# Performance work log

Measured on AMD Instinct MI355X. Metric: run time of the kernel, lower is better.

The kernel has to match this reference:

```python
import jax, jax.numpy as jnp
import numpy as np

NB = 8      # n_blocks
DIM = 256   # model dim (= context_len in source)
DI = 512    # dim_inner = dim * expand(2)
DCONV = 4   # depthwise conv kernel
NS = 16     # d_state
DTR = 16    # dt_rank = ceil(dim/16)
NE = 4      # experts
INNER = 512 # MoE FFN inner = dim * multi(2)
L = 8192    # sequence length
HOR = 32    # horizon
EPS = 1e-3


def setup_inputs() -> dict:
    key = jax.random.key(0)
    ks = jax.random.split(key, 16)
    s = 0.02
    f = lambda k, shp: jax.random.normal(k, shp, jnp.float32) * s
    return {
        "x": jax.random.normal(ks[0], (DIM, L), jnp.float32),
        "lin_w": f(ks[1], (DIM, DIM)),                      # shared by self.linear and self.out (tied)
        "in_proj_w": f(ks[2], (NB, 2 * DI, DIM)),
        "conv_w": f(ks[3], (NB, DI, 1, DCONV)),             # depthwise conv, groups=DI
        "conv_b": f(ks[4], (NB, DI)),
        "x_proj_w": f(ks[5], (NB, DTR + 2 * NS, DI)),
        "dt_proj_w": f(ks[6], (NB, DI, DTR)),
        "dt_proj_b": f(ks[7], (NB, DI)),
        "A_log": jnp.tile(jnp.log(jnp.arange(1, NS + 1, dtype=jnp.float32)), (NB, DI, 1)),
        "D_param": jnp.ones((NB, DI), jnp.float32),
        "out_proj_w": f(ks[8], (NB, DIM, DI)),
        "gate_w": f(ks[9], (NB, NE, DIM)),
        "gproj_w": f(ks[10], (NB, NE, INNER, DIM)),
        "uproj_w": f(ks[11], (NB, NE, INNER, DIM)),
        "dproj_w": f(ks[12], (NB, NE, DIM, INNER)),
        "rms_a_w": jnp.ones((DIM,), jnp.float32),
        "rms_f_w": jnp.ones((DIM,), jnp.float32),
        "head_w1": f(ks[13], (DIM, DIM)),
        "head_w2": f(ks[14], (HOR, DIM)),
    }


def _rmsnorm(h, w):
    return w * (h * jax.lax.rsqrt(jnp.mean(h * h, axis=-1, keepdims=True) + EPS))


def _mamba(h, ipw, cw, cb, xpw, dtw, dtb, alog, dpar, opw):
    b = h.shape[0]
    xr = jnp.einsum('bld,od->bol', h, ipw)            # (b, 2*DI, l)
    xc, res = jnp.split(xr, 2, axis=1)                # each (b, DI, l)
    # causal depthwise conv (padding=DCONV-1, sliced to length l)
    xc = jax.lax.conv_general_dilated(xc, cw, (1,), [(DCONV - 1, 0)],
                                      feature_group_count=DI,
                                      dimension_numbers=('NCH', 'OIH', 'NCH'))
    xc = jax.nn.silu(xc + cb[None, :, None])
    A = -jnp.exp(alog)                                # (DI, NS)
    xdbl = jnp.einsum('bdl,kd->blk', xc, xpw)         # (b, l, DTR+2*NS)
    dr, B, C = xdbl[..., :DTR], xdbl[..., DTR:DTR + NS], xdbl[..., DTR + NS:]
    delta = jax.nn.softplus(jnp.einsum('blr,dr->bld', dr, dtw) + dtb)
    dA = jnp.exp(jnp.einsum('bld,dn->lbdn', delta, A))          # (l, b, DI, NS)
    dBu = jnp.einsum('bld,bln,bdl->lbdn', delta, B, xc)         # (l, b, DI, NS)
    Cl = jnp.transpose(C, (1, 0, 2))                             # (l, b, NS)
    def step(carry, inp):
        a, bu, c = inp
        carry = a * carry + bu
        return carry, jnp.einsum('bdn,bn->bd', carry, c)
    _, ys = jax.lax.scan(step, jnp.zeros((b, DI, NS), xc.dtype), (dA, dBu, Cl))
    y = jnp.transpose(ys, (1, 2, 0)) + xc * dpar[:, None]        # (b, DI, l)
    y = y * jax.nn.silu(res)
    return jnp.einsum('bdl,od->blo', y, opw)                     # (b, l, DIM)


def _moe(h, gw, gp, up, dp):
    shp = h.shape
    xf = h.reshape(-1, shp[-1])                       # (T, DIM)
    scores = xf @ gw.T                                # (T, NE)
    vals, idx = jax.lax.top_k(scores, 2)
    w = jax.nn.softmax(vals, axis=-1)                 # (T, 2)
    g = jax.nn.silu(jnp.einsum('td,ehd->teh', xf, gp))
    u = jnp.einsum('td,ehd->teh', xf, up)
    eo = jnp.einsum('teh,edh->ted', g * u, dp)        # (T, NE, DIM)
    we = jnp.sum(w[..., None] * jax.nn.one_hot(idx, NE, dtype=xf.dtype), axis=1)  # (T, NE)
    return jnp.einsum('te,ted->td', we, eo).reshape(shp)


def reference(x, lin_w, in_proj_w, conv_w, conv_b, x_proj_w, dt_proj_w, dt_proj_b,
              A_log, D_param, out_proj_w, gate_w, gproj_w, uproj_w, dproj_w,
              rms_a_w, rms_f_w, head_w1, head_w2):
    h = x.T[None]                                     # (1, L, DIM)
    h = h @ lin_w.T
    for i in range(NB):
        resi = h
        h = _rmsnorm(h, rms_a_w)
        h = _mamba(h, in_proj_w[i], conv_w[i], conv_b[i], x_proj_w[i],
                   dt_proj_w[i], dt_proj_b[i], A_log[i], D_param[i], out_proj_w[i])
        h = h + resi
        resi = h
        h = _moe(h, gate_w[i], gproj_w[i], uproj_w[i], dproj_w[i])
        h = _rmsnorm(h, rms_f_w)
        h = h + resi
    h = h @ lin_w.T                                   # self.out (tied weight)
    h = jax.nn.silu(h @ head_w1.T) @ head_w2.T        # head
    return jax.nn.sigmoid(h[0].T)                     # (HOR, L)
```

## Files before the change

### kernel.cpp

```cpp
#include <hip/hip_runtime.h>

typedef unsigned short u16;
typedef unsigned int u32;
using bf16x8 = __attribute__((ext_vector_type(8))) short;
using f32x4 = __attribute__((ext_vector_type(4))) float;

constexpr int kL = 8192;
constexpr int kDIM = 256;
constexpr int kDI = 512;
constexpr int kNB = 8;
constexpr float kEPS = 1e-3f;

__device__ __forceinline__ u16 f2b(float f) {
  u32 x = __builtin_bit_cast(u32, f);
  x += 0x7fffu + ((x >> 16) & 1u);
  return (u16)(x >> 16);
}
__device__ __forceinline__ float b2f(u16 u) {
  return __builtin_bit_cast(float, (u32)u << 16);
}
__device__ __forceinline__ float sigm(float x) { return 1.f / (1.f + __expf(-x)); }
__device__ __forceinline__ float softplus_fast(float x) {
  return fmaxf(x, 0.f) + __logf(1.f + __expf(-fabsf(x)));
}

__device__ __forceinline__ void async_cp16(const void* g, void* l) {
  __builtin_amdgcn_global_load_lds((const __attribute__((address_space(1))) u32*)g,
                                   (__attribute__((address_space(3))) u32*)l, 16, 0, 0);
}

struct Cvt2 {
  const float* s[23];
  u16* d[23];
  int n[23];
  int mode[23];
  int bstart[24];
  int nseg;
};
__global__ __launch_bounds__(256) void cvt2_k(Cvt2 dd) {
  const int b = blockIdx.x;
  int seg = 0;
  for (int i = 1; i < dd.nseg; ++i) seg += (b >= dd.bstart[i]) ? 1 : 0;
  const int lb = b - dd.bstart[seg];
  const float* s = dd.s[seg];
  u16* d = dd.d[seg];
  const int n = dd.n[seg];
  const int mode = dd.mode[seg];
  #pragma unroll
  for (int it = 0; it < 4; ++it) {
    const int e4 = lb * 1024 + it * 256 + threadIdx.x;
    const int i = e4 * 4;
    if (i >= n) break;
    const float4 v = ((const float4*)s)[e4];
    ushort4 o = make_ushort4(f2b(v.x), f2b(v.y), f2b(v.z), f2b(v.w));
    size_t dst;
    if (mode == 0) {
      dst = (size_t)i;
    } else if (mode == 1) {
      const int row = i >> 8, col = i & 255;
      const int drow = (row >> 9) * 1024 + ((row >> 4) & 31) * 32 + (row & 15);
      dst = (size_t)drow * 256 + col;
    } else {
      const int bb = i >> 19, e = (i >> 17) & 3, nr = (i >> 9) & 255, j = i & 511;
      dst = (size_t)bb * 524288 + (size_t)nr * 2048 + e * 512 + j;
    }
    *(ushort4*)&d[dst] = o;
  }
}

__global__ __launch_bounds__(256) void transpose_x_k(const float* __restrict__ x, u16* __restrict__ xT) {
  __shared__ float tile[32][33];
  int l0 = blockIdx.x * 32, d0 = blockIdx.y * 32;
  int tx = threadIdx.x, ty = threadIdx.y;
  #pragma unroll
  for (int i = 0; i < 32; i += 8)
    tile[ty + i][tx] = x[(size_t)(d0 + ty + i) * kL + l0 + tx];
  __syncthreads();
  #pragma unroll
  for (int i = 0; i < 32; i += 8)
    xT[(size_t)(l0 + ty + i) * kDIM + d0 + tx] = f2b(tile[tx][ty + i]);
}

template <int BM, int BN, int TR, int TC, int WCN, int MODE>
__global__ __launch_bounds__(256) void gemm_t(
    const u16* __restrict__ A, int lda,
    const u16* __restrict__ W, int ldw,
    void* __restrict__ C, int ldc,
    int N, int K, int pstride)
{
  constexpr int BNR = (BN + 63) & ~63;
  __shared__ u16 As[BM * 64];
  __shared__ u16 Bs[BNR * 64];
  const int tid = threadIdx.x;
  const int lane = tid & 63;
  const int wave = tid >> 6;
  const int bm = blockIdx.x * BM;
  const int bn = blockIdx.y * BN;
  const int wrow = (wave / WCN) * (TR * 16);
  const int wcol = (wave % WCN) * (TC * 16);
  const int kchunk = K / (int)gridDim.z;
  const int kbeg = blockIdx.z * kchunk;
  const int kend = kbeg + kchunk;

  f32x4 acc[TR][TC];
  #pragma unroll
  for (int r = 0; r < TR; ++r)
    #pragma unroll
    for (int c = 0; c < TC; ++c)
      acc[r][c] = f32x4{0.f, 0.f, 0.f, 0.f};

  for (int k0 = kbeg; k0 < kend; k0 += 64) {
    #pragma unroll
    for (int it = 0; it < BM * 64 / 2048; ++it) {
      int flat = (it * 256 + tid) * 8;
      int r = flat >> 6;
      int gc = ((((flat >> 3) & 7) ^ (r & 7)) << 3);
      async_cp16(A + (size_t)(bm + r) * lda + k0 + gc, &As[flat]);
    }
    #pragma unroll
    for (int it = 0; it < BNR * 64 / 2048; ++it) {
      int flat = (it * 256 + tid) * 8;
      int r = flat >> 6;
      int gc = ((((flat >> 3) & 7) ^ (r & 7)) << 3);
      int n = bn + r;
      if (n > N - 1) n = N - 1;
      async_cp16(W + (size_t)n * ldw + k0 + gc, &Bs[flat]);
    }
    __syncthreads();
    #pragma unroll
    for (int kk = 0; kk < 64; kk += 32) {
      const int kc = (kk >> 3) + (lane >> 4);
      const int mrow = lane & 15;
      bf16x8 a[TR], b[TC];
      #pragma unroll
      for (int rr = 0; rr < TR; ++rr) {
        int row = wrow + rr * 16 + mrow;
        a[rr] = *(const bf16x8*)&As[row * 64 + ((kc ^ (row & 7)) << 3)];
      }
      #pragma unroll
      for (int cc = 0; cc < TC; ++cc) {
        int row = wcol + cc * 16 + mrow;
        b[cc] = *(const bf16x8*)&Bs[row * 64 + ((kc ^ (row & 7)) << 3)];
      }
      #pragma unroll
      for (int rr = 0; rr < TR; ++rr)
        #pragma unroll
        for (int cc = 0; cc < TC; ++cc)
          acc[rr][cc] = __builtin_amdgcn_mfma_f32_16x16x32_bf16(a[rr], b[cc], acc[rr][cc], 0, 0, 0);
    }
    __syncthreads();
  }

  const int colb = bn + wcol + (lane & 15);
  const int rowb = bm + wrow + ((lane >> 4) << 2);
  #pragma unroll
  for (int rr = 0; rr < TR; ++rr)
    #pragma unroll
    for (int cc = 0; cc < TC; ++cc) {
      int col = colb + cc * 16;
      if (col >= N) continue;
      #pragma unroll
      for (int i = 0; i < 4; ++i) {
        const int row = rowb + rr * 16 + i;
        size_t off = (size_t)row * ldc + col;
        float v = acc[rr][cc][i];
        if constexpr (MODE == 0) ((float*)C)[off] = v;
        else if constexpr (MODE == 2) ((u16*)C)[off] = f2b(v);
        else if constexpr (MODE == 3) ((u16*)C)[off] = f2b(v * sigm(v));
        else if constexpr (MODE == 4) atomicAdd(&((float*)C)[off], v);
        else if constexpr (MODE == 5) ((float*)C)[off + (size_t)blockIdx.z * pstride] = v;
        else if constexpr (MODE == 7) ((float*)C)[(size_t)col * kL + row] = sigm(v);
      }
    }
}

__global__ __launch_bounds__(512, 1) void moe_mega_k(
    float* __restrict__ h, const float* __restrict__ hpart,
    const float* __restrict__ gw,
    const u16* __restrict__ Wgu, const u16* __restrict__ Wd,
    const float* __restrict__ wf, const float* __restrict__ wa,
    u16* __restrict__ hb2, u16* __restrict__ hn)
{
  __shared__ u16 Ah[32 * 256];
  __shared__ u16 Ts[32 * 512];
  __shared__ u16 Ws[2][256 * 64];
  __shared__ float WeS[32][4];
  const int tid = threadIdx.x;
  const int lane = tid & 63;
  const int quad = lane >> 4;
  const int m16 = lane & 15;
  const int wave = tid >> 6;
  const int wcol = wave * 32;
  const int r0 = blockIdx.x * 32;
  const int prow = tid >> 4;
  const int pcol = (tid & 15) * 16;

  float hv[16];
  {
    const size_t base = (size_t)(r0 + prow) * 256 + pcol;
    #pragma unroll
    for (int j = 0; j < 16; j += 4) {
      float4 v = *(const float4*)(h + base + j);
      #pragma unroll
      for (int z = 0; z < 4; ++z) {
        const float4 pv = *(const float4*)(hpart + (size_t)z * 2097152 + base + j);
        v.x += pv.x; v.y += pv.y; v.z += pv.z; v.w += pv.w;
      }
      hv[j] = v.x; hv[j + 1] = v.y; hv[j + 2] = v.z; hv[j + 3] = v.w;
    }
  }
  {
    float p[4];
    #pragma unroll
    for (int e = 0; e < 4; ++e) {
      float s = 0.f;
      #pragma unroll
      for (int j = 0; j < 16; ++j) s += hv[j] * gw[e * 256 + pcol + j];
      p[e] = s;
    }
    #pragma unroll
    for (int o = 8; o > 0; o >>= 1) {
      p[0] += __shfl_xor(p[0], o); p[1] += __shfl_xor(p[1], o);
      p[2] += __shfl_xor(p[2], o); p[3] += __shfl_xor(p[3], o);
    }
    if ((tid & 15) == 0) {
      int i0 = 0;
      #pragma unroll
      for (int e = 1; e < 4; ++e) if (p[e] > p[i0]) i0 = e;
      int i1 = -1;
      #pragma unroll
      for (int e = 0; e < 4; ++e) {
        if (e == i0) continue;
        if (i1 < 0 || p[e] > p[i1]) i1 = e;
      }
      const float tt = __expf(p[i1] - p[i0]);
      float o0 = 1.f / (1.f + tt), o1 = tt / (1.f + tt);
      WeS[prow][0] = 0.f; WeS[prow][1] = 0.f; WeS[prow][2] = 0.f; WeS[prow][3] = 0.f;
      WeS[prow][i0] = o0; WeS[prow][i1] = o1;
    }
    #pragma unroll
    for (int cc = 0; cc < 2; ++cc) {
      const int chunk = (pcol >> 3) + cc;
      const int sw = ((chunk ^ (prow & 7)) << 3);
      u16 tmp[8];
      #pragma unroll
      for (int j = 0; j < 8; ++j) tmp[j] = f2b(hv[cc * 8 + j]);
      *(bf16x8*)&Ah[prow * 256 + sw] = *(bf16x8*)tmp;
    }
  }
  __syncthreads();

  f32x4 macc[2][2];
  #pragma unroll
  for (int rt = 0; rt < 2; ++rt)
    #pragma unroll
    for (int ct = 0; ct < 2; ++ct) macc[rt][ct] = f32x4{0.f, 0.f, 0.f, 0.f};

  auto stage_gu = [&](int buf, int e, int nc, int k0) {
    #pragma unroll
    for (int it = 0; it < 4; ++it) {
      const int flat = (it * 512 + tid) * 8;
      const int r = flat >> 6;
      const int gc = ((((flat >> 3) & 7) ^ (r & 7)) << 3);
      async_cp16(Wgu + (size_t)(e * 1024 + nc * 256 + r) * 256 + k0 + gc, &Ws[buf][flat]);
    }
  };
  auto stage_dp = [&](int buf, int e, int k0) {
    #pragma unroll
    for (int it = 0; it < 4; ++it) {
      const int flat = (it * 512 + tid) * 8;
      const int r = flat >> 6;
      const int gc = ((((flat >> 3) & 7) ^ (r & 7)) << 3);
      async_cp16(Wd + (size_t)r * 2048 + e * 512 + k0 + gc, &Ws[buf][flat]);
    }
  };

  for (int e = 0; e < 4; ++e) {
    for (int nc = 0; nc < 4; ++nc) {
      f32x4 acc[2][2];
      #pragma unroll
      for (int rt = 0; rt < 2; ++rt)
        #pragma unroll
        for (int ct = 0; ct < 2; ++ct) acc[rt][ct] = f32x4{0.f, 0.f, 0.f, 0.f};
      stage_gu(0, e, nc, 0);
      __syncthreads();
      #pragma unroll
      for (int k0i = 0; k0i < 4; ++k0i) {
        if (k0i < 3) stage_gu((k0i + 1) & 1, e, nc, (k0i + 1) * 64);
        const u16* buf = Ws[k0i & 1];
        #pragma unroll
        for (int kk = 0; kk < 64; kk += 32) {
          const int kcs = (kk >> 3) + quad;
          bf16x8 a[2], b[2];
          #pragma unroll
          for (int rt = 0; rt < 2; ++rt) {
            const int row = rt * 16 + m16;
            const int ch = ((k0i * 64 + kk) >> 3) + quad;
            a[rt] = *(const bf16x8*)&Ah[row * 256 + ((ch ^ (row & 7)) << 3)];
          }
          #pragma unroll
          for (int ct = 0; ct < 2; ++ct) {
            const int n = wcol + ct * 16 + m16;
            b[ct] = *(const bf16x8*)&buf[n * 64 + ((kcs ^ (n & 7)) << 3)];
          }
          #pragma unroll
          for (int rt = 0; rt < 2; ++rt)
            #pragma unroll
            for (int ct = 0; ct < 2; ++ct)
              acc[rt][ct] = __builtin_amdgcn_mfma_f32_16x16x32_bf16(a[rt], b[ct], acc[rt][ct], 0, 0, 0);
        }
        __syncthreads();
      }
      const int group = nc * 8 + wave;
      const int j = group * 16 + m16;
      #pragma unroll
      for (int rt = 0; rt < 2; ++rt)
        #pragma unroll
        for (int i = 0; i < 4; ++i) {
          const int row = rt * 16 + quad * 4 + i;
          const float g = acc[rt][0][i];
          const float u = acc[rt][1][i];
          const float val = g * sigm(g) * u * WeS[row][e];
          Ts[row * 512 + (((j >> 3) ^ (row & 7)) << 3) + (j & 7)] = f2b(val);
        }
    }
    __syncthreads();
    stage_dp(0, e, 0);
    __syncthreads();
    #pragma unroll
    for (int k0i = 0; k0i < 8; ++k0i) {
      if (k0i < 7) stage_dp((k0i + 1) & 1, e, (k0i + 1) * 64);
      const u16* buf = Ws[k0i & 1];
      #pragma unroll
      for (int kk = 0; kk < 64; kk += 32) {
        const int kcs = (kk >> 3) + quad;
        bf16x8 a[2], b[2];
        #pragma unroll
        for (int rt = 0; rt < 2; ++rt) {
          const int row = rt * 16 + m16;
          const int ch = ((k0i * 64 + kk) >> 3) + quad;
          a[rt] = *(const bf16x8*)&Ts[row * 512 + ((ch ^ (row & 7)) << 3)];
        }
        #pragma unroll
        for (int ct = 0; ct < 2; ++ct) {
          const int n = wcol + ct * 16 + m16;
          b[ct] = *(const bf16x8*)&buf[n * 64 + ((kcs ^ (n & 7)) << 3)];
        }
        #pragma unroll
        for (int rt = 0; rt < 2; ++rt)
          #pragma unroll
          for (int ct = 0; ct < 2; ++ct)
            macc[rt][ct] = __builtin_amdgcn_mfma_f32_16x16x32_bf16(a[rt], b[ct], macc[rt][ct], 0, 0, 0);
      }
      __syncthreads();
    }
  }

  float* MoeS = (float*)Ts;
  __syncthreads();
  #pragma unroll
  for (int rt = 0; rt < 2; ++rt)
    #pragma unroll
    for (int ct = 0; ct < 2; ++ct)
      #pragma unroll
      for (int i = 0; i < 4; ++i)
        MoeS[(rt * 16 + quad * 4 + i) * 256 + wcol + ct * 16 + m16] = macc[rt][ct][i];
  __syncthreads();

  float mv[16];
  float ss = 0.f;
  #pragma unroll
  for (int j = 0; j < 16; ++j) {
    mv[j] = MoeS[prow * 256 + pcol + j];
    ss += mv[j] * mv[j];
  }
  #pragma unroll
  for (int o = 8; o > 0; o >>= 1) ss += __shfl_xor(ss, o);
  const float r1 = rsqrtf(ss * (1.f / 256.f) + kEPS);
  float ss2 = 0.f;
  #pragma unroll
  for (int j = 0; j < 16; ++j) {
    hv[j] += wf[pcol + j] * mv[j] * r1;
    ss2 += hv[j] * hv[j];
  }
  #pragma unroll
  for (int o = 8; o > 0; o >>= 1) ss2 += __shfl_xor(ss2, o);
  const float r2 = rsqrtf(ss2 * (1.f / 256.f) + kEPS);

  const size_t base = (size_t)(r0 + prow) * 256 + pcol;
  #pragma unroll
  for (int j = 0; j < 16; j += 4)
    *(float4*)(h + base + j) = float4{hv[j], hv[j + 1], hv[j + 2], hv[j + 3]};
  #pragma unroll
  for (int j = 0; j < 16; j += 4) {
    *(ushort4*)(hb2 + base + j) = make_ushort4(f2b(hv[j]), f2b(hv[j + 1]), f2b(hv[j + 2]), f2b(hv[j + 3]));
    *(ushort4*)(hn + base + j) = make_ushort4(
        f2b(wa[pcol + j] * hv[j] * r2), f2b(wa[pcol + j + 1] * hv[j + 1] * r2),
        f2b(wa[pcol + j + 2] * hv[j + 2] * r2), f2b(wa[pcol + j + 3] * hv[j + 3] * r2));
  }
}

__device__ __forceinline__ float block_sum256(float v) {
  #pragma unroll
  for (int o = 32; o > 0; o >>= 1) v += __shfl_down(v, o);
  __shared__ float red[4];
  __syncthreads();
  if ((threadIdx.x & 63) == 0) red[threadIdx.x >> 6] = v;
  __syncthreads();
  return red[0] + red[1] + red[2] + red[3];
}

__global__ __launch_bounds__(256) void rms_a_k(const float* __restrict__ h, const float* __restrict__ w,
                                               u16* __restrict__ hn) {
  const int l = blockIdx.x, t = threadIdx.x;
  const float v = h[(size_t)l * kDIM + t];
  const float ssum = block_sum256(v * v);
  const float r = rsqrtf(ssum * (1.f / 256.f) + kEPS);
  hn[(size_t)l * kDIM + t] = f2b(w[t] * v * r);
}

__global__ __launch_bounds__(256) void conv_silu_k(const u16* __restrict__ xz, const float* __restrict__ cw,
                                                   const float* __restrict__ cb,
                                                   u16* __restrict__ xcb, u16* __restrict__ zsb,
                                                   float* __restrict__ xdbl) {
  const int i4 = blockIdx.x * 256 + threadIdx.x;
  if (i4 < 98304) *(float4*)&xdbl[i4 * 4] = float4{0.f, 0.f, 0.f, 0.f};
  const int l = i4 >> 7;
  const int d = (i4 & 127) * 4;
  float acc[4];
  const float4 cbv = *(const float4*)&cb[d];
  acc[0] = cbv.x; acc[1] = cbv.y; acc[2] = cbv.z; acc[3] = cbv.w;
  #pragma unroll
  for (int j = 0; j < 4; ++j) {
    const int ll = l - 3 + j;
    if (ll >= 0) {
      const ushort4 xv = *(const ushort4*)&xz[(size_t)ll * 1024 + d];
      acc[0] += cw[(d + 0) * 4 + j] * b2f(xv.x);
      acc[1] += cw[(d + 1) * 4 + j] * b2f(xv.y);
      acc[2] += cw[(d + 2) * 4 + j] * b2f(xv.z);
      acc[3] += cw[(d + 3) * 4 + j] * b2f(xv.w);
    }
  }
  ushort4 xo, zo;
  const ushort4 zv = *(const ushort4*)&xz[(size_t)l * 1024 + 512 + d];
  float z0 = b2f(zv.x), z1 = b2f(zv.y), z2 = b2f(zv.z), z3 = b2f(zv.w);
  xo.x = f2b(acc[0] * sigm(acc[0])); xo.y = f2b(acc[1] * sigm(acc[1]));
  xo.z = f2b(acc[2] * sigm(acc[2])); xo.w = f2b(acc[3] * sigm(acc[3]));
  zo.x = f2b(z0 * sigm(z0)); zo.y = f2b(z1 * sigm(z1));
  zo.z = f2b(z2 * sigm(z2)); zo.w = f2b(z3 * sigm(z3));
  *(ushort4*)&xcb[(size_t)l * 512 + d] = xo;
  *(ushort4*)&zsb[(size_t)l * 512 + d] = zo;
}

__global__ __launch_bounds__(256) void scan_a_k(const float* __restrict__ xdbl, const u16* __restrict__ xcb,
                                                const float* __restrict__ A_log, const float* __restrict__ dtw,
                                                const float* __restrict__ dtb,
                                                u16* __restrict__ delta,
                                                float* __restrict__ aprod, float* __restrict__ bacc) {
  const int c = blockIdx.x;
  const int t = threadIdx.x;
  const int half = t & 1;
  const int d = blockIdx.y * 128 + (t >> 1);
  const int l0 = c * 64;
  __shared__ float Xs[64][32];
  for (int i = t; i < 2048; i += 256)
    Xs[i >> 5][i & 31] = xdbl[(size_t)(l0 + (i >> 5)) * 48 + (i & 31)];
  __syncthreads();
  float wd[8], Ad[8];
  #pragma unroll
  for (int j = 0; j < 8; ++j) wd[j] = dtw[d * 16 + half * 8 + j];
  const float bd = dtb[d];
  #pragma unroll
  for (int n = 0; n < 8; ++n) Ad[n] = -__expf(A_log[d * 16 + half * 8 + n]);
  float s[8], ap[8];
  #pragma unroll
  for (int n = 0; n < 8; ++n) { s[n] = 0.f; ap[n] = 1.f; }
  #pragma unroll 4
  for (int lr = 0; lr < 64; ++lr) {
    const float4 dr0 = *(const float4*)&Xs[lr][half * 8];
    const float4 dr1 = *(const float4*)&Xs[lr][half * 8 + 4];
    float p0 = dr0.x * wd[0] + dr0.y * wd[1] + dr0.z * wd[2] + dr0.w * wd[3];
    float p1 = dr1.x * wd[4] + dr1.y * wd[5] + dr1.z * wd[6] + dr1.w * wd[7];
    float dot = p0 + p1;
    dot += __shfl_xor(dot, 1);
    const float dl = softplus_fast(dot + bd);
    const int l = l0 + lr;
    if (!half) delta[(size_t)l * 512 + d] = f2b(dl);
    const float du = dl * b2f(xcb[(size_t)l * 512 + d]);
    const float4 B0 = *(const float4*)&Xs[lr][16 + half * 8];
    const float4 B1 = *(const float4*)&Xs[lr][16 + half * 8 + 4];
    const float Bv[8] = {B0.x, B0.y, B0.z, B0.w, B1.x, B1.y, B1.z, B1.w};
    #pragma unroll
    for (int n = 0; n < 8; ++n) {
      const float a = __expf(dl * Ad[n]);
      s[n] = fmaf(a, s[n], du * Bv[n]);
      ap[n] *= a;
    }
  }
  const int base = c * 8192 + d * 16 + half * 8;
  #pragma unroll
  for (int n = 0; n < 8; ++n) { aprod[base + n] = ap[n]; bacc[base + n] = s[n]; }
}

__global__ __launch_bounds__(256) void scan_b_k(const float* __restrict__ aprod, const float* __restrict__ bacc,
                                                float* __restrict__ sinit) {
  const int st = blockIdx.x * 256 + threadIdx.x;
  float cur = 0.f;
  float a0 = aprod[st], b0 = bacc[st];
  for (int c = 0; c < 128; ++c) {
    float a1 = 0.f, b1 = 0.f;
    if (c + 1 < 128) {
      a1 = aprod[(size_t)(c + 1) * 8192 + st];
      b1 = bacc[(size_t)(c + 1) * 8192 + st];
    }
    sinit[(size_t)c * 8192 + st] = cur;
    cur = fmaf(a0, cur, b0);
    a0 = a1; b0 = b1;
  }
}

__global__ __launch_bounds__(256) void scan_c_k(const float* __restrict__ xdbl, const u16* __restrict__ xcb,
                                                const u16* __restrict__ zsb, const float* __restrict__ A_log,
                                                const u16* __restrict__ delta,
                                                const float* __restrict__ sinit,
                                                const float* __restrict__ Dp, u16* __restrict__ yv) {
  const int c = blockIdx.x;
  const int t = threadIdx.x;
  const int half = t & 1;
  const int d = blockIdx.y * 128 + (t >> 1);
  const int l0 = c * 64;
  __shared__ float Xs[64][32];
  for (int i = t; i < 2048; i += 256)
    Xs[i >> 5][i & 31] = xdbl[(size_t)(l0 + (i >> 5)) * 48 + 16 + (i & 31)];
  __syncthreads();
  float Ad[8];
  #pragma unroll
  for (int n = 0; n < 8; ++n) Ad[n] = -__expf(A_log[d * 16 + half * 8 + n]);
  float s[8];
  const int base = c * 8192 + d * 16 + half * 8;
  #pragma unroll
  for (int n = 0; n < 8; ++n) s[n] = sinit[base + n];
  const float Dd = Dp[d];
  #pragma unroll 4
  for (int lr = 0; lr < 64; ++lr) {
    const int l = l0 + lr;
    const float dl = b2f(delta[(size_t)l * 512 + d]);
    const float xv = b2f(xcb[(size_t)l * 512 + d]);
    const float zs = b2f(zsb[(size_t)l * 512 + d]);
    const float du = dl * xv;
    const float4 B0 = *(const float4*)&Xs[lr][half * 8];
    const float4 B1 = *(const float4*)&Xs[lr][half * 8 + 4];
    const float4 C0 = *(const float4*)&Xs[lr][16 + half * 8];
    const float4 C1 = *(const float4*)&Xs[lr][16 + half * 8 + 4];
    const float Bv[8] = {B0.x, B0.y, B0.z, B0.w, B1.x, B1.y, B1.z, B1.w};
    const float Cv[8] = {C0.x, C0.y, C0.z, C0.w, C1.x, C1.y, C1.z, C1.w};
    float y = 0.f;
    #pragma unroll
    for (int n = 0; n < 8; ++n) {
      const float a = __expf(dl * Ad[n]);
      s[n] = fmaf(a, s[n], du * Bv[n]);
      y = fmaf(s[n], Cv[n], y);
    }
    y += __shfl_xor(y, 1);
    if (!half) yv[(size_t)l * 512 + d] = f2b((y + xv * Dd) * zs);
  }
}

extern "C" void kernel_launch(void* const* d_in, const int* in_sizes, int n_in,
                              void* d_out, int out_size, void* d_ws, size_t ws_size,
                              hipStream_t stream) {
  const float* x        = (const float*)d_in[0];
  const float* lin_w    = (const float*)d_in[1];
  const float* in_proj  = (const float*)d_in[2];
  const float* conv_w   = (const float*)d_in[3];
  const float* conv_b   = (const float*)d_in[4];
  const float* x_proj   = (const float*)d_in[5];
  const float* dt_w     = (const float*)d_in[6];
  const float* dt_b     = (const float*)d_in[7];
  const float* A_log    = (const float*)d_in[8];
  const float* D_param  = (const float*)d_in[9];
  const float* out_proj = (const float*)d_in[10];
  const float* gate_w   = (const float*)d_in[11];
  const float* gproj    = (const float*)d_in[12];
  const float* uproj    = (const float*)d_in[13];
  const float* dproj    = (const float*)d_in[14];
  const float* rms_a_w  = (const float*)d_in[15];
  const float* rms_f_w  = (const float*)d_in[16];
  const float* head_w1  = (const float*)d_in[17];
  const float* head_w2  = (const float*)d_in[18];

  char* p = (char*)d_ws;
  auto alloc = [&](size_t bytes) -> char* {
    char* r = p;
    p += (bytes + 255) & ~(size_t)255;
    return r;
  };

  u16* lin_b  = (u16*)alloc(65536 * 2);
  u16* ipw_b  = (u16*)alloc((size_t)2097152 * 2);
  u16* xpw_b  = (u16*)alloc((size_t)196608 * 2);
  u16* opw_b  = (u16*)alloc((size_t)1048576 * 2);
  u16* gupw_b = (u16*)alloc((size_t)8388608 * 2);
  u16* dpw_b  = (u16*)alloc((size_t)4194304 * 2);
  u16* hw1_b  = (u16*)alloc(65536 * 2);
  u16* hw2_b  = (u16*)alloc(8192 * 2);

  u16* xT     = (u16*)alloc((size_t)kL * kDIM * 2);
  float* h    = (float*)alloc((size_t)kL * kDIM * 4);
  u16* hn     = (u16*)alloc((size_t)kL * kDIM * 2);
  u16* hb2    = (u16*)alloc((size_t)kL * kDIM * 2);
  float* xdbl = (float*)alloc((size_t)kL * 48 * 4);
  u16* fb     = (u16*)alloc((size_t)kL * kDIM * 2);
  u16* h2b    = (u16*)alloc((size_t)kL * kDIM * 2);
  u16* xz     = (u16*)alloc((size_t)kL * 1024 * 2);
  u16* xcb    = (u16*)alloc((size_t)kL * kDI * 2);
  u16* zsb    = (u16*)alloc((size_t)kL * kDI * 2);
  u16* yv     = (u16*)alloc((size_t)kL * kDI * 2);
  u16* delta  = (u16*)alloc((size_t)kL * kDI * 2);
  float* aprod = (float*)alloc((size_t)128 * 8192 * 4);
  float* bacc  = (float*)alloc((size_t)128 * 8192 * 4);
  float* sinit = (float*)alloc((size_t)128 * 8192 * 4);
  float* hpart = (float*)alloc((size_t)4 * kL * kDIM * 4);

  if ((size_t)(p - (char*)d_ws) > ws_size) return;

  Cvt2 dd;
  int seg = 0, blk = 0;
  auto add = [&](const float* s, u16* d, int n, int mode) {
    dd.s[seg] = s; dd.d[seg] = d; dd.n[seg] = n; dd.mode[seg] = mode;
    dd.bstart[seg] = blk;
    blk += (n + 4095) / 4096;
    ++seg;
  };
  add(lin_w, lin_b, 65536, 0);
  add(in_proj, ipw_b, 2097152, 0);
  add(x_proj, xpw_b, 196608, 0);
  add(out_proj, opw_b, 1048576, 0);
  add(head_w1, hw1_b, 65536, 0);
  add(head_w2, hw2_b, 8192, 0);
  for (int i = 0; i < kNB; ++i) {
    add(gproj + (size_t)i * 524288, gupw_b + (size_t)i * 1048576, 524288, 1);
    add(uproj + (size_t)i * 524288, gupw_b + (size_t)i * 1048576 + 4096, 524288, 1);
  }
  add(dproj, dpw_b, 4194304, 2);
  dd.nseg = seg;
  dd.bstart[seg] = blk;
  cvt2_k<<<blk, 256, 0, stream>>>(dd);
  transpose_x_k<<<dim3(kL / 32, kDIM / 32), dim3(32, 8), 0, stream>>>(x, xT);

  gemm_t<64, 128, 2, 4, 2, 0><<<dim3(128, 2, 1), 256, 0, stream>>>(
      xT, 256, lin_b, 256, h, 256, 256, 256, 0);
  rms_a_k<<<kL, 256, 0, stream>>>(h, rms_a_w, hn);

  for (int i = 0; i < kNB; ++i) {
    gemm_t<128, 128, 4, 4, 2, 2><<<dim3(64, 8, 1), 256, 0, stream>>>(
        hn, 256, ipw_b + (size_t)i * 262144, 256, xz, 1024, 1024, 256, 0);
    conv_silu_k<<<kL * kDI / 1024, 256, 0, stream>>>(xz, conv_w + (size_t)i * 2048,
                                                     conv_b + (size_t)i * 512, xcb, zsb, xdbl);
    gemm_t<128, 48, 2, 3, 1, 4><<<dim3(64, 1, 8), 256, 0, stream>>>(
        xcb, 512, xpw_b + (size_t)i * 24576, 512, xdbl, 48, 48, 512, 0);
    scan_a_k<<<dim3(128, 4), 256, 0, stream>>>(xdbl, xcb, A_log + (size_t)i * 8192,
                                               dt_w + (size_t)i * 8192, dt_b + (size_t)i * 512,
                                               delta, aprod, bacc);
    scan_b_k<<<32, 256, 0, stream>>>(aprod, bacc, sinit);
    scan_c_k<<<dim3(128, 4), 256, 0, stream>>>(xdbl, xcb, zsb, A_log + (size_t)i * 8192,
                                               delta, sinit, D_param + (size_t)i * 512, yv);
    gemm_t<128, 128, 4, 4, 2, 5><<<dim3(64, 2, 4), 256, 0, stream>>>(
        yv, 512, opw_b + (size_t)i * 131072, 512, hpart, 256, 256, 512, 2097152);
    moe_mega_k<<<256, 512, 0, stream>>>(h, hpart, gate_w + (size_t)i * 1024,
                                        gupw_b + (size_t)i * 1048576, dpw_b + (size_t)i * 524288,
                                        rms_f_w, rms_a_w, hb2, hn);
  }

  gemm_t<64, 128, 2, 4, 2, 2><<<dim3(128, 2, 1), 256, 0, stream>>>(
      hb2, 256, lin_b, 256, h2b, 256, 256, 256, 0);
  gemm_t<64, 128, 2, 4, 2, 3><<<dim3(128, 2, 1), 256, 0, stream>>>(
      h2b, 256, hw1_b, 256, fb, 256, 256, 256, 0);
  gemm_t<64, 128, 2, 4, 2, 7><<<dim3(128, 1, 1), 256, 0, stream>>>(
      fb, 256, hw2_b, 256, (float*)d_out, 32, 32, 256, 0);
}
```

Measured before the change: 2.147 ms.

## Load MoE expert weights directly from global memory instead of LDS staging

Drops the double-buffered LDS staging of the gate/up and down-projection weight tiles in the fused MoE kernel. Each wave now reads its B fragments straight from global memory, which removes many block-wide barriers and 64KB of shared memory. Launch bounds are raised to allow up to four blocks per CU for more occupancy. The trade-off is uncoalesced, strided global loads with no cross-wave reuse: every block re-reads all expert weights and must rely on the L2 cache, and latency hiding now depends on occupancy rather than async prefetch.

```diff
diff --git a/kernel.cpp b/kernel.cpp
--- a/kernel.cpp
+++ b/kernel.cpp
@@ -174,7 +174,7 @@
     }
 }
 
-__global__ __launch_bounds__(512, 1) void moe_mega_k(
+__global__ __launch_bounds__(512, 4) void moe_mega_k(
     float* __restrict__ h, const float* __restrict__ hpart,
     const float* __restrict__ gw,
     const u16* __restrict__ Wgu, const u16* __restrict__ Wd,
@@ -183,14 +183,12 @@
 {
   __shared__ u16 Ah[32 * 256];
   __shared__ u16 Ts[32 * 512];
-  __shared__ u16 Ws[2][256 * 64];
   __shared__ float WeS[32][4];
   const int tid = threadIdx.x;
   const int lane = tid & 63;
   const int quad = lane >> 4;
   const int m16 = lane & 15;
   const int wave = tid >> 6;
-  const int wcol = wave * 32;
   const int r0 = blockIdx.x * 32;
   const int prow = tid >> 4;
   const int pcol = (tid & 15) * 16;
@@ -256,60 +254,32 @@
     #pragma unroll
     for (int ct = 0; ct < 2; ++ct) macc[rt][ct] = f32x4{0.f, 0.f, 0.f, 0.f};
 
-  auto stage_gu = [&](int buf, int e, int nc, int k0) {
-    #pragma unroll
-    for (int it = 0; it < 4; ++it) {
-      const int flat = (it * 512 + tid) * 8;
-      const int r = flat >> 6;
-      const int gc = ((((flat >> 3) & 7) ^ (r & 7)) << 3);
-      async_cp16(Wgu + (size_t)(e * 1024 + nc * 256 + r) * 256 + k0 + gc, &Ws[buf][flat]);
-    }
-  };
-  auto stage_dp = [&](int buf, int e, int k0) {
-    #pragma unroll
-    for (int it = 0; it < 4; ++it) {
-      const int flat = (it * 512 + tid) * 8;
-      const int r = flat >> 6;
-      const int gc = ((((flat >> 3) & 7) ^ (r & 7)) << 3);
-      async_cp16(Wd + (size_t)r * 2048 + e * 512 + k0 + gc, &Ws[buf][flat]);
-    }
-  };
-
   for (int e = 0; e < 4; ++e) {
+    #pragma unroll
     for (int nc = 0; nc < 4; ++nc) {
       f32x4 acc[2][2];
       #pragma unroll
       for (int rt = 0; rt < 2; ++rt)
         #pragma unroll
         for (int ct = 0; ct < 2; ++ct) acc[rt][ct] = f32x4{0.f, 0.f, 0.f, 0.f};
-      stage_gu(0, e, nc, 0);
-      __syncthreads();
-      #pragma unroll
-      for (int k0i = 0; k0i < 4; ++k0i) {
-        if (k0i < 3) stage_gu((k0i + 1) & 1, e, nc, (k0i + 1) * 64);
-        const u16* buf = Ws[k0i & 1];
+      const u16* wbase = Wgu + (size_t)(e * 1024 + nc * 256 + wave * 32) * 256;
+      #pragma unroll
+      for (int k0 = 0; k0 < 256; k0 += 32) {
+        const int ch = (k0 >> 3) + quad;
+        bf16x8 a[2], b[2];
         #pragma unroll
-        for (int kk = 0; kk < 64; kk += 32) {
-          const int kcs = (kk >> 3) + quad;
-          bf16x8 a[2], b[2];
+        for (int rt = 0; rt < 2; ++rt) {
+          const int row = rt * 16 + m16;
+          a[rt] = *(const bf16x8*)&Ah[row * 256 + ((ch ^ (row & 7)) << 3)];
+        }
+        #pragma unroll
+        for (int ct = 0; ct < 2; ++ct)
+          b[ct] = *(const bf16x8*)&wbase[(ct * 16 + m16) * 256 + k0 + quad * 8];
+        #pragma unroll
+        for (int rt = 0; rt < 2; ++rt)
           #pragma unroll
-          for (int rt = 0; rt < 2; ++rt) {
-            const int row = rt * 16 + m16;
-            const int ch = ((k0i * 64 + kk) >> 3) + quad;
-            a[rt] = *(const bf16x8*)&Ah[row * 256 + ((ch ^ (row & 7)) << 3)];
-          }
-          #pragma unroll
-          for (int ct = 0; ct < 2; ++ct) {
-            const int n = wcol + ct * 16 + m16;
-            b[ct] = *(const bf16x8*)&buf[n * 64 + ((kcs ^ (n & 7)) << 3)];
-          }
-          #pragma unroll
-          for (int rt = 0; rt < 2; ++rt)
-            #pragma unroll
-            for (int ct = 0; ct < 2; ++ct)
-              acc[rt][ct] = __builtin_amdgcn_mfma_f32_16x16x32_bf16(a[rt], b[ct], acc[rt][ct], 0, 0, 0);
-        }
-        __syncthreads();
+          for (int ct = 0; ct < 2; ++ct)
+            acc[rt][ct] = __builtin_amdgcn_mfma_f32_16x16x32_bf16(a[rt], b[ct], acc[rt][ct], 0, 0, 0);
       }
       const int group = nc * 8 + wave;
       const int j = group * 16 + m16;
@@ -325,46 +295,36 @@
         }
     }
     __syncthreads();
-    stage_dp(0, e, 0);
+    const u16* dbase = Wd + (size_t)(wave * 32) * 2048 + e * 512;
+    #pragma unroll
+    for (int k0 = 0; k0 < 512; k0 += 32) {
+      const int ch = (k0 >> 3) + quad;
+      bf16x8 a[2], b[2];
+      #pragma unroll
+      for (int rt = 0; rt < 2; ++rt) {
+        const int row = rt * 16 + m16;
+        a[rt] = *(const bf16x8*)&Ts[row * 512 + ((ch ^ (row & 7)) << 3)];
+      }
+      #pragma unroll
+      for (int ct = 0; ct < 2; ++ct)
+        b[ct] = *(const bf16x8*)&dbase[(ct * 16 + m16) * 2048 + k0 + quad * 8];
+      #pragma unroll
+      for (int rt = 0; rt < 2; ++rt)
+        #pragma unroll
+        for (int ct = 0; ct < 2; ++ct)
+          macc[rt][ct] = __builtin_amdgcn_mfma_f32_16x16x32_bf16(a[rt], b[ct], macc[rt][ct], 0, 0, 0);
+    }
     __syncthreads();
-    #pragma unroll
-    for (int k0i = 0; k0i < 8; ++k0i) {
-      if (k0i < 7) stage_dp((k0i + 1) & 1, e, (k0i + 1) * 64);
-      const u16* buf = Ws[k0i & 1];
-      #pragma unroll
-      for (int kk = 0; kk < 64; kk += 32) {
-        const int kcs = (kk >> 3) + quad;
-        bf16x8 a[2], b[2];
-        #pragma unroll
-        for (int rt = 0; rt < 2; ++rt) {
-          const int row = rt * 16 + m16;
-          const int ch = ((k0i * 64 + kk) >> 3) + quad;
-          a[rt] = *(const bf16x8*)&Ts[row * 512 + ((ch ^ (row & 7)) << 3)];
-        }
-        #pragma unroll
-        for (int ct = 0; ct < 2; ++ct) {
-          const int n = wcol + ct * 16 + m16;
-          b[ct] = *(const bf16x8*)&buf[n * 64 + ((kcs ^ (n & 7)) << 3)];
-        }
-        #pragma unroll
-        for (int rt = 0; rt < 2; ++rt)
-          #pragma unroll
-          for (int ct = 0; ct < 2; ++ct)
-            macc[rt][ct] = __builtin_amdgcn_mfma_f32_16x16x32_bf16(a[rt], b[ct], macc[rt][ct], 0, 0, 0);
-      }
-      __syncthreads();
-    }
   }
 
   float* MoeS = (float*)Ts;
-  __syncthreads();
   #pragma unroll
   for (int rt = 0; rt < 2; ++rt)
     #pragma unroll
     for (int ct = 0; ct < 2; ++ct)
       #pragma unroll
       for (int i = 0; i < 4; ++i)
-        MoeS[(rt * 16 + quad * 4 + i) * 256 + wcol + ct * 16 + m16] = macc[rt][ct][i];
+        MoeS[(rt * 16 + quad * 4 + i) * 256 + wave * 32 + ct * 16 + m16] = macc[rt][ct][i];
   __syncthreads();
 
   float mv[16];
```

After: 2.835 ms. 32.1% more time.
